# Kernel optimization log

Measured on AMD Instinct MI355X. Metric: run time of the kernel, lower is better.

## Reference

```python
import jax, jax.numpy as jnp
import numpy as np

D_MODEL = 768
NUM_HEADS = 12
SEQ_LEN = 4096
BATCH = 1


def setup_inputs() -> dict:
    key = jax.random.key(0)
    k1, k2, k3, k4 = jax.random.split(key, 4)
    x = jax.random.normal(k1, (BATCH, SEQ_LEN, D_MODEL), dtype=jnp.float32)
    # nn.Linear(d_model, 3*d_model, bias=False): store as [d_model, 3*d_model] so h = x @ w_qkv
    w_qkv = jax.random.normal(k2, (D_MODEL, 3 * D_MODEL), dtype=jnp.float32) * (1.0 / np.sqrt(D_MODEL))
    w_proj = jax.random.normal(k3, (D_MODEL, D_MODEL), dtype=jnp.float32) * (1.0 / np.sqrt(D_MODEL))
    b_proj = jax.random.normal(k4, (D_MODEL,), dtype=jnp.float32) * 0.01
    return {"x": x, "w_qkv": w_qkv, "w_proj": w_proj, "b_proj": b_proj}


def reference(x, w_qkv, w_proj, b_proj):
    n, t, c = x.shape
    H = NUM_HEADS
    dh = c // H
    # fused QKV projection: [n, t, 3c] -> per head contiguous [q|k|v] chunks of dh
    h = (x @ w_qkv).reshape(n, t, H, 3, dh)
    q = h[..., 0, :]  # [n, t, H, dh]
    k = h[..., 1, :]
    v = h[..., 2, :]
    scale = 1.0 / np.sqrt(dh)
    # full TxT score matrix, as in the hand-rolled torch module
    scores = jnp.einsum('nqhd,nkhd->nhqk', q, k) * scale  # [n, H, t, t]
    causal = jnp.tril(jnp.ones((t, t), dtype=bool))  # tril buffer
    scores = jnp.where(causal, scores, jnp.finfo(scores.dtype).min)
    att = jax.nn.softmax(scores, axis=-1)
    out = jnp.einsum('nhqk,nkhd->nqhd', att, v).reshape(n, t, c)
    return out @ w_proj + b_proj
```

## Files before the change

kernel.cpp:

```cpp
#include <hip/hip_runtime.h>

#define T_SEQ 4096
#define DM    768
#define NH    12
#define DH    64
#define NC    2304

using half8  = __attribute__((ext_vector_type(8))) _Float16;
using half4v = __attribute__((ext_vector_type(4))) _Float16;
using f32x4  = __attribute__((ext_vector_type(4))) float;
using f32x16 = __attribute__((ext_vector_type(16))) float;
typedef unsigned int u32;

union H8 { half8 v; u32 u[4]; };

__device__ __forceinline__ u32 pkrtz_u32(float a, float b) {
    return __builtin_bit_cast(u32, __builtin_amdgcn_cvt_pkrtz(a, b));
}
__device__ __forceinline__ float asf(u32 x) { return __builtin_bit_cast(float, x); }
__device__ __forceinline__ u32 asu(float x) { return __builtin_bit_cast(u32, x); }

__device__ __forceinline__ void async_copy16(void* lds, const void* g) {
    __builtin_amdgcn_global_load_lds(
        (const __attribute__((address_space(1))) u32*)g,
        (__attribute__((address_space(3))) u32*)lds, 16, 0, 0);
}

__global__ __launch_bounds__(256)
void convert_x_kernel(const float* __restrict__ x, _Float16* __restrict__ xh) {
    const size_t i = ((size_t)blockIdx.x * 256 + threadIdx.x) * 8;
    float4 a = *(const float4*)(x + i);
    float4 b = *(const float4*)(x + i + 4);
    half8 o = { (_Float16)a.x, (_Float16)a.y, (_Float16)a.z, (_Float16)a.w,
                (_Float16)b.x, (_Float16)b.y, (_Float16)b.z, (_Float16)b.w };
    *(half8*)(xh + i) = o;
}

__global__ __launch_bounds__(256)
void transpose_convert_kernel(const float* __restrict__ src,
                              _Float16* __restrict__ dst, int R, int C) {
    __shared__ _Float16 tile[64][72];
    const int tid = threadIdx.x;
    const int tc0 = blockIdx.x * 64;
    const int tr0 = blockIdx.y * 64;
    const int r = tid >> 2, c4 = (tid & 3) * 16;
    const float* sp = src + (size_t)(tr0 + r) * C + tc0 + c4;
    #pragma unroll
    for (int j = 0; j < 16; j += 4) {
        float4 t4 = *(const float4*)(sp + j);
        tile[r][c4 + j + 0] = (_Float16)t4.x;
        tile[r][c4 + j + 1] = (_Float16)t4.y;
        tile[r][c4 + j + 2] = (_Float16)t4.z;
        tile[r][c4 + j + 3] = (_Float16)t4.w;
    }
    __syncthreads();
    const int c = tid >> 2, r4 = (tid & 3) * 16;
    half8 o0, o1;
    #pragma unroll
    for (int j = 0; j < 8; ++j) o0[j] = tile[r4 + j][c];
    #pragma unroll
    for (int j = 0; j < 8; ++j) o1[j] = tile[r4 + 8 + j][c];
    _Float16* dp = dst + (size_t)(tc0 + c) * R + tr0 + r4;
    *(half8*)(dp) = o0;
    *(half8*)(dp + 8) = o1;
}

__global__ __launch_bounds__(256, 2)
void qkv_mfma_kernel(const _Float16* __restrict__ A,
                     const _Float16* __restrict__ Bt,
                     _Float16* __restrict__ q, _Float16* __restrict__ k,
                     _Float16* __restrict__ vt) {
    __shared__ _Float16 Alds[128 * 64];
    __shared__ _Float16 Blds[128 * 64];
    const int tid  = threadIdx.x;
    const int lane = tid & 63;
    const int w    = tid >> 6;
    const int wr = w >> 1, wc = w & 1;
    const int lrow = lane >> 4, lcol = lane & 15;

    const int bid  = blockIdx.x;
    const int virt = (bid & 7) * 72 + (bid >> 3);
    const int cbn  = virt % 18, rbn = virt / 18;

    const _Float16* Ag = A  + (size_t)rbn * 128 * DM;
    const _Float16* Bg = Bt + (size_t)cbn * 128 * DM;

    int srow[4], scol[4];
    #pragma unroll
    for (int i = 0; i < 4; ++i) {
        const int idx = i * 256 + tid;
        srow[i] = idx >> 3;
        scol[i] = ((idx & 7) ^ (srow[i] & 7)) * 8;
    }

    f32x4 acc[4][4];
    #pragma unroll
    for (int mf = 0; mf < 4; ++mf)
        #pragma unroll
        for (int nf = 0; nf < 4; ++nf) acc[mf][nf] = (f32x4){0.f, 0.f, 0.f, 0.f};

    for (int kt = 0; kt < DM / 64; ++kt) {
        const int k0 = kt * 64;
        __syncthreads();
        #pragma unroll
        for (int i = 0; i < 4; ++i) {
            async_copy16((char*)Alds + (i * 256 + w * 64) * 16,
                         Ag + (size_t)srow[i] * DM + k0 + scol[i]);
            async_copy16((char*)Blds + (i * 256 + w * 64) * 16,
                         Bg + (size_t)srow[i] * DM + k0 + scol[i]);
        }
        __syncthreads();
        #pragma unroll
        for (int kh = 0; kh < 2; ++kh) {
            half8 af[4], bf[4];
            const int ag = kh * 4 + lrow;
            #pragma unroll
            for (int f = 0; f < 4; ++f) {
                const int ar = wr * 64 + f * 16 + lcol;
                af[f] = *(const half8*)((const char*)Alds +
                          ar * 128 + ((ag ^ (ar & 7)) << 4));
                const int br = wc * 64 + f * 16 + lcol;
                bf[f] = *(const half8*)((const char*)Blds +
                          br * 128 + ((ag ^ (br & 7)) << 4));
            }
            #pragma unroll
            for (int mf = 0; mf < 4; ++mf)
                #pragma unroll
                for (int nf = 0; nf < 4; ++nf)
                    acc[mf][nf] = __builtin_amdgcn_mfma_f32_16x16x32_f16(
                        af[mf], bf[nf], acc[mf][nf], 0, 0, 0);
        }
    }

    #pragma unroll
    for (int nf = 0; nf < 4; ++nf) {
        const int n = cbn * 128 + wc * 64 + nf * 16 + lcol;
        const int head  = n / 192;
        const int which = (n >> 6) % 3;
        const int d = n & 63;
        if (which == 2) {
            _Float16* dv = vt + ((size_t)head * DH + d) * T_SEQ;
            #pragma unroll
            for (int mf = 0; mf < 4; ++mf) {
                const int t0 = rbn * 128 + wr * 64 + mf * 16 + lrow * 4;
                half4v o = { (_Float16)acc[mf][nf][0], (_Float16)acc[mf][nf][1],
                             (_Float16)acc[mf][nf][2], (_Float16)acc[mf][nf][3] };
                *(half4v*)(dv + t0) = o;
            }
        } else {
            _Float16* dst = (which == 0) ? q : k;
            const float sc = (which == 0) ? 0.18033688011112042f : 1.0f;
            dst += (size_t)head * T_SEQ * DH + d;
            #pragma unroll
            for (int mf = 0; mf < 4; ++mf) {
                const int t0 = rbn * 128 + wr * 64 + mf * 16 + lrow * 4;
                #pragma unroll
                for (int r = 0; r < 4; ++r)
                    dst[(size_t)(t0 + r) * DH] = (_Float16)(acc[mf][nf][r] * sc);
            }
        }
    }
}

__global__ __launch_bounds__(256, 2)
void proj_mfma_kernel(const _Float16* __restrict__ A,
                      const _Float16* __restrict__ Bt,
                      const float* __restrict__ bias, float* __restrict__ out) {
    __shared__ _Float16 Alds[128 * 64];
    __shared__ _Float16 Blds[128 * 64];
    const int tid  = threadIdx.x;
    const int lane = tid & 63;
    const int w    = tid >> 6;
    const int wr = w >> 1, wc = w & 1;
    const int lrow = lane >> 4, lcol = lane & 15;

    const int bid  = blockIdx.x;
    const int virt = (bid & 7) * 24 + (bid >> 3);
    const int cbn  = virt % 6, rbn = virt / 6;

    const _Float16* Ag = A  + (size_t)rbn * 128 * DM;
    const _Float16* Bg = Bt + (size_t)cbn * 128 * DM;

    int srow[4], scol[4];
    #pragma unroll
    for (int i = 0; i < 4; ++i) {
        const int idx = i * 256 + tid;
        srow[i] = idx >> 3;
        scol[i] = ((idx & 7) ^ (srow[i] & 7)) * 8;
    }

    f32x4 acc[4][4];
    #pragma unroll
    for (int mf = 0; mf < 4; ++mf)
        #pragma unroll
        for (int nf = 0; nf < 4; ++nf) acc[mf][nf] = (f32x4){0.f, 0.f, 0.f, 0.f};

    for (int kt = 0; kt < DM / 64; ++kt) {
        const int k0 = kt * 64;
        __syncthreads();
        #pragma unroll
        for (int i = 0; i < 4; ++i) {
            async_copy16((char*)Alds + (i * 256 + w * 64) * 16,
                         Ag + (size_t)srow[i] * DM + k0 + scol[i]);
            async_copy16((char*)Blds + (i * 256 + w * 64) * 16,
                         Bg + (size_t)srow[i] * DM + k0 + scol[i]);
        }
        __syncthreads();
        #pragma unroll
        for (int kh = 0; kh < 2; ++kh) {
            half8 af[4], bf[4];
            const int ag = kh * 4 + lrow;
            #pragma unroll
            for (int f = 0; f < 4; ++f) {
                const int ar = wr * 64 + f * 16 + lcol;
                af[f] = *(const half8*)((const char*)Alds +
                          ar * 128 + ((ag ^ (ar & 7)) << 4));
                const int br = wc * 64 + f * 16 + lcol;
                bf[f] = *(const half8*)((const char*)Blds +
                          br * 128 + ((ag ^ (br & 7)) << 4));
            }
            #pragma unroll
            for (int mf = 0; mf < 4; ++mf)
                #pragma unroll
                for (int nf = 0; nf < 4; ++nf)
                    acc[mf][nf] = __builtin_amdgcn_mfma_f32_16x16x32_f16(
                        af[mf], bf[nf], acc[mf][nf], 0, 0, 0);
        }
    }

    #pragma unroll
    for (int nf = 0; nf < 4; ++nf) {
        const int n = cbn * 128 + wc * 64 + nf * 16 + lcol;
        const float b = bias[n];
        #pragma unroll
        for (int mf = 0; mf < 4; ++mf) {
            const int t0 = rbn * 128 + wr * 64 + mf * 16 + lrow * 4;
            #pragma unroll
            for (int r = 0; r < 4; ++r)
                out[(size_t)(t0 + r) * DM + n] = acc[mf][nf][r] + b;
        }
    }
}

__global__ __launch_bounds__(256, 2)
void attn_tile_kernel(const _Float16* __restrict__ qg,
                      const _Float16* __restrict__ kg,
                      const _Float16* __restrict__ vtg,
                      _Float16* __restrict__ pO,
                      float* __restrict__ pml) {
    __shared__ _Float16 Kl[3][4096];
    __shared__ _Float16 Vl[3][4096];

    const int tid  = threadIdx.x;
    const int lane = tid & 63;
    const int w    = tid >> 6;
    const int l31  = lane & 31;
    const int hi   = lane >> 5;

    const int b = blockIdx.x;
    const int h = b % NH;
    const int i = 39 - b / NH;
    int j, seg;
    if (i < 4)       { j = i;                 seg = 0; }
    else if (i < 12) { const int t = i - 4;   j = 4  + (t >> 1); seg = t & 1; }
    else if (i < 24) { const int t = i - 12;  j = 8  + t / 3;    seg = t % 3; }
    else             { const int t = i - 24;  j = 12 + (t >> 2); seg = t & 3; }

    const int c0 = 8 * j + w;
    const int c1 = 8 * j + 4 + w;
    const int q0 = c0 * 32 + l31;
    const int q1 = c1 * 32 + l31;
    const int niter0 = c0 / 2 + 1;
    const int niter1 = c1 / 2 + 1;
    const int tS      = seg * 16;
    const int tEndBlk = min(tS + 16, 4 * j + 4);
    const int tEnd0   = min(tS + 16, niter0);
    const int tEnd1   = min(tS + 16, niter1);

    const _Float16* Kh = kg  + (size_t)h * T_SEQ * DH;
    const _Float16* Vh = vtg + (size_t)h * DH * T_SEQ;

    half8 qf0[4], qf1[4];
    {
        const _Float16* Q0 = qg + ((size_t)h * T_SEQ + q0) * DH + hi * 8;
        const _Float16* Q1 = qg + ((size_t)h * T_SEQ + q1) * DH + hi * 8;
        #pragma unroll
        for (int ks = 0; ks < 4; ++ks) {
            qf0[ks] = *(const half8*)(Q0 + ks * 16);
            qf1[ks] = *(const half8*)(Q1 + ks * 16);
        }
    }

    f32x16 oA0 = {}, oA1 = {};
    f32x16 oB0 = {}, oB1 = {};
    float l0 = 0.f, l1 = 0.f;

    const int g0 = tid, g1 = tid + 256;
    const int r0 = g0 >> 3, s0 = ((g0 & 7) ^ (r0 & 7)) * 8;
    const int r1 = g1 >> 3, s1 = ((g1 & 7) ^ (r1 & 7)) * 8;

    auto stage = [&](int p, int kvb) {
        async_copy16((char*)Kl[p] + g0 * 16, Kh + (size_t)(kvb + r0) * DH + s0);
        async_copy16((char*)Kl[p] + g1 * 16, Kh + (size_t)(kvb + r1) * DH + s1);
        async_copy16((char*)Vl[p] + g0 * 16, Vh + (size_t)r0 * T_SEQ + kvb + s0);
        async_copy16((char*)Vl[p] + g1 * 16, Vh + (size_t)r1 * T_SEQ + kvb + s1);
    };

    stage(0, tS * 64);
    stage(1, min(tS + 1, tEndBlk - 1) * 64);
    stage(2, min(tS + 2, tEndBlk - 1) * 64);

    for (int it = tS; it < tEndBlk; ++it) {
        const int p = (it - tS) % 3;

        if (it + 2 < tEndBlk) {
            asm volatile("s_waitcnt vmcnt(8)" ::: "memory");
        } else if (it + 1 < tEndBlk) {
            asm volatile("s_waitcnt vmcnt(4)" ::: "memory");
        } else {
            asm volatile("s_waitcnt vmcnt(0)" ::: "memory");
        }
        __builtin_amdgcn_s_barrier();

        if (it < tEnd1) {
            const int kvb = it * 64;
            const char* Kb = (const char*)Kl[p];
            const char* Vb = (const char*)Vl[p];
            const int sw7 = l31 & 7;

            half8 kfA[4], kfB[4];
            #pragma unroll
            for (int ks = 0; ks < 4; ++ks) {
                const int gsl = (ks * 2 + hi) ^ sw7;
                kfA[ks] = *(const half8*)(Kb + l31 * 128 + (gsl << 4));
                kfB[ks] = *(const half8*)(Kb + (32 + l31) * 128 + (gsl << 4));
            }
            half8 vf[2][2][2];
            #pragma unroll
            for (int t = 0; t < 2; ++t)
                #pragma unroll
                for (int dt = 0; dt < 2; ++dt)
                    #pragma unroll
                    for (int ks2 = 0; ks2 < 2; ++ks2) {
                        const int gsl = (t * 4 + ks2 * 2 + hi) ^ sw7;
                        vf[t][dt][ks2] = *(const half8*)(Vb +
                            (dt * 32 + l31) * 128 + (gsl << 4));
                    }

            auto run_stream = [&](const half8* qf, f32x16& o0v, f32x16& o1v,
                                  float& lsum, int qrow, int niter) {
                f32x16 sA, sB;
                #pragma unroll
                for (int r = 0; r < 16; ++r) { sA[r] = -8.0f; sB[r] = -8.0f; }
                __builtin_amdgcn_s_setprio(1);
                #pragma unroll
                for (int ks = 0; ks < 4; ++ks) {
                    sA = __builtin_amdgcn_mfma_f32_32x32x16_f16(kfA[ks], qf[ks], sA, 0, 0, 0);
                    sB = __builtin_amdgcn_mfma_f32_32x32x16_f16(kfB[ks], qf[ks], sB, 0, 0, 0);
                }
                __builtin_amdgcn_s_setprio(0);

                if (it == niter - 1) {
                    #pragma unroll
                    for (int r = 0; r < 16; ++r) {
                        const int off = (r & 3) + 8 * (r >> 2) + 4 * hi;
                        if (kvb + off > qrow)      sA[r] = -1e30f;
                        if (kvb + 32 + off > qrow) sB[r] = -1e30f;
                    }
                }

                #pragma unroll
                for (int r = 0; r < 16; ++r) sA[r] = __builtin_amdgcn_exp2f(sA[r]);
                #pragma unroll
                for (int r = 0; r < 16; ++r) sB[r] = __builtin_amdgcn_exp2f(sB[r]);
                float s8[8];
                #pragma unroll
                for (int r = 0; r < 8; ++r)
                    s8[r] = (sA[r] + sA[r + 8]) + (sB[r] + sB[r + 8]);
                float rsum = ((s8[0] + s8[4]) + (s8[1] + s8[5])) +
                             ((s8[2] + s8[6]) + (s8[3] + s8[7]));
                {
                    auto rr = __builtin_amdgcn_permlane32_swap(asu(rsum), asu(rsum), false, false);
                    rsum = asf(rr[0]) + asf(rr[1]);
                }
                lsum += rsum;

                H8 pfA[2], pfB[2];
                #pragma unroll
                for (int ks2 = 0; ks2 < 2; ++ks2) {
                    {
                        const u32 a0 = pkrtz_u32(sA[8*ks2+0], sA[8*ks2+1]);
                        const u32 a1 = pkrtz_u32(sA[8*ks2+2], sA[8*ks2+3]);
                        const u32 b0 = pkrtz_u32(sA[8*ks2+4], sA[8*ks2+5]);
                        const u32 b1 = pkrtz_u32(sA[8*ks2+6], sA[8*ks2+7]);
                        auto r0v = __builtin_amdgcn_permlane32_swap(a0, b0, false, false);
                        auto r1v = __builtin_amdgcn_permlane32_swap(a1, b1, false, false);
                        pfA[ks2].u[0] = r0v[0];
                        pfA[ks2].u[1] = r1v[0];
                        pfA[ks2].u[2] = r0v[1];
                        pfA[ks2].u[3] = r1v[1];
                    }
                    {
                        const u32 a0 = pkrtz_u32(sB[8*ks2+0], sB[8*ks2+1]);
                        const u32 a1 = pkrtz_u32(sB[8*ks2+2], sB[8*ks2+3]);
                        const u32 b0 = pkrtz_u32(sB[8*ks2+4], sB[8*ks2+5]);
                        const u32 b1 = pkrtz_u32(sB[8*ks2+6], sB[8*ks2+7]);
                        auto r0v = __builtin_amdgcn_permlane32_swap(a0, b0, false, false);
                        auto r1v = __builtin_amdgcn_permlane32_swap(a1, b1, false, false);
                        pfB[ks2].u[0] = r0v[0];
                        pfB[ks2].u[1] = r1v[0];
                        pfB[ks2].u[2] = r0v[1];
                        pfB[ks2].u[3] = r1v[1];
                    }
                }

                __builtin_amdgcn_s_setprio(1);
                #pragma unroll
                for (int ks2 = 0; ks2 < 2; ++ks2) {
                    o0v = __builtin_amdgcn_mfma_f32_32x32x16_f16(vf[0][0][ks2], pfA[ks2].v, o0v, 0, 0, 0);
                    o1v = __builtin_amdgcn_mfma_f32_32x32x16_f16(vf[0][1][ks2], pfA[ks2].v, o1v, 0, 0, 0);
                    o0v = __builtin_amdgcn_mfma_f32_32x32x16_f16(vf[1][0][ks2], pfB[ks2].v, o0v, 0, 0, 0);
                    o1v = __builtin_amdgcn_mfma_f32_32x32x16_f16(vf[1][1][ks2], pfB[ks2].v, o1v, 0, 0, 0);
                }
                __builtin_amdgcn_s_setprio(0);
            };

            if (it < tEnd0) run_stream(qf0, oA0, oA1, l0, q0, niter0);
            run_stream(qf1, oB0, oB1, l1, q1, niter1);
        }

        __builtin_amdgcn_s_barrier();
        if (it + 3 < tEndBlk) stage(p, (it + 3) * 64);
    }

    auto write_partial = [&](int c, const f32x16& o0v, const f32x16& o1v, float l) {
        const int hc = h * 128 + c;
        const float inv = (l > 0.f) ? 1.0f / l : 0.f;
        _Float16* op = pO + ((size_t)(seg * 1536 + hc) * 32 + l31) * 64 + 4 * hi;
        #pragma unroll
        for (int g = 0; g < 4; ++g) {
            half4v w0 = { (_Float16)(o0v[4*g+0] * inv), (_Float16)(o0v[4*g+1] * inv),
                          (_Float16)(o0v[4*g+2] * inv), (_Float16)(o0v[4*g+3] * inv) };
            half4v w1 = { (_Float16)(o1v[4*g+0] * inv), (_Float16)(o1v[4*g+1] * inv),
                          (_Float16)(o1v[4*g+2] * inv), (_Float16)(o1v[4*g+3] * inv) };
            *(half4v*)(op + 8 * g)      = w0;
            *(half4v*)(op + 32 + 8 * g) = w1;
        }
        if (hi == 0) {
            float* mp = pml + ((size_t)(seg * 1536 + hc) * 32 + l31) * 2;
            mp[0] = 0.0f;
            mp[1] = l;
        }
    };
    write_partial(c0, oA0, oA1, l0);
    write_partial(c1, oB0, oB1, l1);
}

__global__ __launch_bounds__(256)
void attn_combine_kernel(const _Float16* __restrict__ pO,
                         const float* __restrict__ pml,
                         _Float16* __restrict__ att) {
    const int row = blockIdx.x * 256 + threadIdx.x;
    const int q5 = row & 31;
    const int hc = row >> 5;
    const int c  = hc & 127;
    const int h  = hc >> 7;
    const int nseg = c / 32 + 1;

    float ll[4];
    float L = 0.f;
    #pragma unroll
    for (int s = 0; s < 4; ++s) {
        const bool on = s < nseg;
        const float* mp = pml + ((size_t)(s * 1536 + hc) * 32 + q5) * 2;
        ll[s] = on ? mp[1] : 0.f;
        L += ll[s];
    }
    const float invL = 1.0f / L;

    float acc[64];
    #pragma unroll
    for (int d = 0; d < 64; ++d) acc[d] = 0.f;
    #pragma unroll
    for (int s = 0; s < 4; ++s) {
        if (s >= nseg) break;
        const _Float16* src = pO + ((size_t)(s * 1536 + hc) * 32 + q5) * 64;
        const float wsc = ll[s] * invL;
        #pragma unroll
        for (int g = 0; g < 8; ++g) {
            half8 v = *(const half8*)(src + g * 8);
            #pragma unroll
            for (int jj = 0; jj < 8; ++jj)
                acc[g * 8 + jj] += wsc * (float)v[jj];
        }
    }
    _Float16* dst = att + (size_t)(c * 32 + q5) * DM + h * DH;
    #pragma unroll
    for (int g = 0; g < 8; ++g) {
        half8 o;
        #pragma unroll
        for (int jj = 0; jj < 8; ++jj) o[jj] = (_Float16)acc[g * 8 + jj];
        *(half8*)(dst + g * 8) = o;
    }
}

extern "C" void kernel_launch(void* const* d_in, const int* in_sizes, int n_in,
                              void* d_out, int out_size, void* d_ws, size_t ws_size,
                              hipStream_t stream) {
    const float* x      = (const float*)d_in[0];
    const float* w_qkv  = (const float*)d_in[1];
    const float* w_proj = (const float*)d_in[2];
    const float* b_proj = (const float*)d_in[3];
    float* out = (float*)d_out;

    _Float16* wsb = (_Float16*)d_ws;
    const size_t XS = (size_t)T_SEQ * DM;
    const size_t HS = (size_t)NH * T_SEQ * DH;
    _Float16* xh     = wsb;
    _Float16* wqkvT  = xh + XS;
    _Float16* wprojT = wqkvT + (size_t)NC * DM;
    _Float16* q      = wprojT + (size_t)DM * DM;
    _Float16* k      = q + HS;
    _Float16* vt     = k + HS;
    _Float16* att    = vt + HS;
    _Float16* pO     = att + XS;
    float*    pml    = (float*)(pO + (size_t)4 * 1536 * 32 * 64);

    convert_x_kernel<<<dim3(1536), 256, 0, stream>>>(x, xh);
    transpose_convert_kernel<<<dim3(36, 12), 256, 0, stream>>>(w_qkv, wqkvT, DM, NC);
    transpose_convert_kernel<<<dim3(12, 12), 256, 0, stream>>>(w_proj, wprojT, DM, DM);
    qkv_mfma_kernel<<<dim3(576), 256, 0, stream>>>(xh, wqkvT, q, k, vt);
    attn_tile_kernel<<<dim3(480), 256, 0, stream>>>(q, k, vt, pO, pml);
    attn_combine_kernel<<<dim3(192), 256, 0, stream>>>(pO, pml, att);
    proj_mfma_kernel<<<dim3(192), 256, 0, stream>>>(att, wprojT, b_proj, out);
}
```

Baseline: 104.9 us.

## Merge prep kernels and retile QKV and projection GEMMs for better wave fill

Folds the x conversion and both weight transposes into a single prep kernel, removing two launches. Changes the QKV GEMM to 128x192 tiles over 384 blocks so each block covers one head's q|k|v columns and reuses A across more columns. Halves the projection GEMM row tile to 64, doubling its grid to 384 blocks to fill more CUs. This adds LDS and accumulator register pressure in the QKV kernel, and the smaller projection tile reuses each B tile across fewer rows.

Measured after the change: 97.17 us (median of 2 runs). -7.4%, faster.

```diff
diff --git a/kernel.cpp b/kernel.cpp
--- a/kernel.cpp
+++ b/kernel.cpp
@@ -27,22 +27,35 @@
 }
 
 __global__ __launch_bounds__(256)
-void convert_x_kernel(const float* __restrict__ x, _Float16* __restrict__ xh) {
-    const size_t i = ((size_t)blockIdx.x * 256 + threadIdx.x) * 8;
-    float4 a = *(const float4*)(x + i);
-    float4 b = *(const float4*)(x + i + 4);
-    half8 o = { (_Float16)a.x, (_Float16)a.y, (_Float16)a.z, (_Float16)a.w,
-                (_Float16)b.x, (_Float16)b.y, (_Float16)b.z, (_Float16)b.w };
-    *(half8*)(xh + i) = o;
-}
-
-__global__ __launch_bounds__(256)
-void transpose_convert_kernel(const float* __restrict__ src,
-                              _Float16* __restrict__ dst, int R, int C) {
+void prep_kernel(const float* __restrict__ x, _Float16* __restrict__ xh,
+                 const float* __restrict__ w_qkv, _Float16* __restrict__ wqkvT,
+                 const float* __restrict__ w_proj, _Float16* __restrict__ wprojT) {
     __shared__ _Float16 tile[64][72];
+    const int b = blockIdx.x;
     const int tid = threadIdx.x;
-    const int tc0 = blockIdx.x * 64;
-    const int tr0 = blockIdx.y * 64;
+
+    if (b < 1536) {
+        const size_t i = ((size_t)b * 256 + tid) * 8;
+        float4 a = *(const float4*)(x + i);
+        float4 c = *(const float4*)(x + i + 4);
+        half8 o = { (_Float16)a.x, (_Float16)a.y, (_Float16)a.z, (_Float16)a.w,
+                    (_Float16)c.x, (_Float16)c.y, (_Float16)c.z, (_Float16)c.w };
+        *(half8*)(xh + i) = o;
+        return;
+    }
+
+    const float* src;
+    _Float16* dst;
+    int R, C, tc0, tr0;
+    if (b < 1968) {
+        const int b2 = b - 1536;
+        src = w_qkv; dst = wqkvT; R = DM; C = NC;
+        tc0 = (b2 % 36) * 64; tr0 = (b2 / 36) * 64;
+    } else {
+        const int b3 = b - 1968;
+        src = w_proj; dst = wprojT; R = DM; C = DM;
+        tc0 = (b3 % 12) * 64; tr0 = (b3 / 12) * 64;
+    }
     const int r = tid >> 2, c4 = (tid & 3) * 16;
     const float* sp = src + (size_t)(tr0 + r) * C + tc0 + c4;
     #pragma unroll
@@ -71,6 +84,112 @@
                      _Float16* __restrict__ q, _Float16* __restrict__ k,
                      _Float16* __restrict__ vt) {
     __shared__ _Float16 Alds[128 * 64];
+    __shared__ _Float16 Blds[192 * 64];
+    const int tid  = threadIdx.x;
+    const int lane = tid & 63;
+    const int w    = tid >> 6;
+    const int wr = w >> 1, wc = w & 1;
+    const int lrow = lane >> 4, lcol = lane & 15;
+
+    const int bid  = blockIdx.x;
+    const int virt = (bid & 7) * 48 + (bid >> 3);
+    const int cbn  = virt % 12, rbn = virt / 12;
+
+    const _Float16* Ag = A  + (size_t)rbn * 128 * DM;
+    const _Float16* Bg = Bt + (size_t)cbn * 192 * DM;
+
+    int srA[4], scA[4], srB[6], scB[6];
+    #pragma unroll
+    for (int i = 0; i < 4; ++i) {
+        const int idx = i * 256 + tid;
+        srA[i] = idx >> 3;
+        scA[i] = ((idx & 7) ^ (srA[i] & 7)) * 8;
+    }
+    #pragma unroll
+    for (int i = 0; i < 6; ++i) {
+        const int idx = i * 256 + tid;
+        srB[i] = idx >> 3;
+        scB[i] = ((idx & 7) ^ (srB[i] & 7)) * 8;
+    }
+
+    f32x4 acc[4][6];
+    #pragma unroll
+    for (int mf = 0; mf < 4; ++mf)
+        #pragma unroll
+        for (int nf = 0; nf < 6; ++nf) acc[mf][nf] = (f32x4){0.f, 0.f, 0.f, 0.f};
+
+    for (int kt = 0; kt < DM / 64; ++kt) {
+        const int k0 = kt * 64;
+        __syncthreads();
+        #pragma unroll
+        for (int i = 0; i < 4; ++i)
+            async_copy16((char*)Alds + (i * 256 + tid) * 16,
+                         Ag + (size_t)srA[i] * DM + k0 + scA[i]);
+        #pragma unroll
+        for (int i = 0; i < 6; ++i)
+            async_copy16((char*)Blds + (i * 256 + tid) * 16,
+                         Bg + (size_t)srB[i] * DM + k0 + scB[i]);
+        __syncthreads();
+        #pragma unroll
+        for (int kh = 0; kh < 2; ++kh) {
+            half8 af[4], bf[6];
+            const int ag = kh * 4 + lrow;
+            #pragma unroll
+            for (int f = 0; f < 4; ++f) {
+                const int ar = wr * 64 + f * 16 + lcol;
+                af[f] = *(const half8*)((const char*)Alds +
+                          ar * 128 + ((ag ^ (ar & 7)) << 4));
+            }
+            #pragma unroll
+            for (int f = 0; f < 6; ++f) {
+                const int br = wc * 96 + f * 16 + lcol;
+                bf[f] = *(const half8*)((const char*)Blds +
+                          br * 128 + ((ag ^ (br & 7)) << 4));
+            }
+            #pragma unroll
+            for (int mf = 0; mf < 4; ++mf)
+                #pragma unroll
+                for (int nf = 0; nf < 6; ++nf)
+                    acc[mf][nf] = __builtin_amdgcn_mfma_f32_16x16x32_f16(
+                        af[mf], bf[nf], acc[mf][nf], 0, 0, 0);
+        }
+    }
+
+    #pragma unroll
+    for (int nf = 0; nf < 6; ++nf) {
+        const int n = cbn * 192 + wc * 96 + nf * 16 + lcol;
+        const int head  = n / 192;
+        const int which = (n >> 6) % 3;
+        const int d = n & 63;
+        if (which == 2) {
+            _Float16* dv = vt + ((size_t)head * DH + d) * T_SEQ;
+            #pragma unroll
+            for (int mf = 0; mf < 4; ++mf) {
+                const int t0 = rbn * 128 + wr * 64 + mf * 16 + lrow * 4;
+                half4v o = { (_Float16)acc[mf][nf][0], (_Float16)acc[mf][nf][1],
+                             (_Float16)acc[mf][nf][2], (_Float16)acc[mf][nf][3] };
+                *(half4v*)(dv + t0) = o;
+            }
+        } else {
+            _Float16* dst = (which == 0) ? q : k;
+            const float sc = (which == 0) ? 0.18033688011112042f : 1.0f;
+            dst += (size_t)head * T_SEQ * DH + d;
+            #pragma unroll
+            for (int mf = 0; mf < 4; ++mf) {
+                const int t0 = rbn * 128 + wr * 64 + mf * 16 + lrow * 4;
+                #pragma unroll
+                for (int r = 0; r < 4; ++r)
+                    dst[(size_t)(t0 + r) * DH] = (_Float16)(acc[mf][nf][r] * sc);
+            }
+        }
+    }
+}
+
+__global__ __launch_bounds__(256, 2)
+void proj_mfma_kernel(const _Float16* __restrict__ A,
+                      const _Float16* __restrict__ Bt,
+                      const float* __restrict__ bias, float* __restrict__ out) {
+    __shared__ _Float16 Alds[64 * 64];
     __shared__ _Float16 Blds[128 * 64];
     const int tid  = threadIdx.x;
     const int lane = tid & 63;
@@ -79,23 +198,29 @@
     const int lrow = lane >> 4, lcol = lane & 15;
 
     const int bid  = blockIdx.x;
-    const int virt = (bid & 7) * 72 + (bid >> 3);
-    const int cbn  = virt % 18, rbn = virt / 18;
-
-    const _Float16* Ag = A  + (size_t)rbn * 128 * DM;
+    const int virt = (bid & 7) * 48 + (bid >> 3);
+    const int cbn  = virt % 6, rbn = virt / 6;
+
+    const _Float16* Ag = A  + (size_t)rbn * 64 * DM;
     const _Float16* Bg = Bt + (size_t)cbn * 128 * DM;
 
-    int srow[4], scol[4];
+    int srA[2], scA[2], srB[4], scB[4];
+    #pragma unroll
+    for (int i = 0; i < 2; ++i) {
+        const int idx = i * 256 + tid;
+        srA[i] = idx >> 3;
+        scA[i] = ((idx & 7) ^ (srA[i] & 7)) * 8;
+    }
     #pragma unroll
     for (int i = 0; i < 4; ++i) {
         const int idx = i * 256 + tid;
-        srow[i] = idx >> 3;
-        scol[i] = ((idx & 7) ^ (srow[i] & 7)) * 8;
-    }
-
-    f32x4 acc[4][4];
-    #pragma unroll
-    for (int mf = 0; mf < 4; ++mf)
+        srB[i] = idx >> 3;
+        scB[i] = ((idx & 7) ^ (srB[i] & 7)) * 8;
+    }
+
+    f32x4 acc[2][4];
+    #pragma unroll
+    for (int mf = 0; mf < 2; ++mf)
         #pragma unroll
         for (int nf = 0; nf < 4; ++nf) acc[mf][nf] = (f32x4){0.f, 0.f, 0.f, 0.f};
 
@@ -103,28 +228,32 @@
         const int k0 = kt * 64;
         __syncthreads();
         #pragma unroll
-        for (int i = 0; i < 4; ++i) {
-            async_copy16((char*)Alds + (i * 256 + w * 64) * 16,
-                         Ag + (size_t)srow[i] * DM + k0 + scol[i]);
-            async_copy16((char*)Blds + (i * 256 + w * 64) * 16,
-                         Bg + (size_t)srow[i] * DM + k0 + scol[i]);
-        }
+        for (int i = 0; i < 2; ++i)
+            async_copy16((char*)Alds + (i * 256 + tid) * 16,
+                         Ag + (size_t)srA[i] * DM + k0 + scA[i]);
+        #pragma unroll
+        for (int i = 0; i < 4; ++i)
+            async_copy16((char*)Blds + (i * 256 + tid) * 16,
+                         Bg + (size_t)srB[i] * DM + k0 + scB[i]);
         __syncthreads();
         #pragma unroll
         for (int kh = 0; kh < 2; ++kh) {
-            half8 af[4], bf[4];
+            half8 af[2], bf[4];
             const int ag = kh * 4 + lrow;
             #pragma unroll
-            for (int f = 0; f < 4; ++f) {
-                const int ar = wr * 64 + f * 16 + lcol;
+            for (int f = 0; f < 2; ++f) {
+                const int ar = wr * 32 + f * 16 + lcol;
                 af[f] = *(const half8*)((const char*)Alds +
                           ar * 128 + ((ag ^ (ar & 7)) << 4));
+            }
+            #pragma unroll
+            for (int f = 0; f < 4; ++f) {
                 const int br = wc * 64 + f * 16 + lcol;
                 bf[f] = *(const half8*)((const char*)Blds +
                           br * 128 + ((ag ^ (br & 7)) << 4));
             }
             #pragma unroll
-            for (int mf = 0; mf < 4; ++mf)
+            for (int mf = 0; mf < 2; ++mf)
                 #pragma unroll
                 for (int nf = 0; nf < 4; ++nf)
                     acc[mf][nf] = __builtin_amdgcn_mfma_f32_16x16x32_f16(
@@ -135,106 +264,10 @@
     #pragma unroll
     for (int nf = 0; nf < 4; ++nf) {
         const int n = cbn * 128 + wc * 64 + nf * 16 + lcol;
-        const int head  = n / 192;
-        const int which = (n >> 6) % 3;
-        const int d = n & 63;
-        if (which == 2) {
-            _Float16* dv = vt + ((size_t)head * DH + d) * T_SEQ;
-            #pragma unroll
-            for (int mf = 0; mf < 4; ++mf) {
-                const int t0 = rbn * 128 + wr * 64 + mf * 16 + lrow * 4;
-                half4v o = { (_Float16)acc[mf][nf][0], (_Float16)acc[mf][nf][1],
-                             (_Float16)acc[mf][nf][2], (_Float16)acc[mf][nf][3] };
-                *(half4v*)(dv + t0) = o;
-            }
-        } else {
-            _Float16* dst = (which == 0) ? q : k;
-            const float sc = (which == 0) ? 0.18033688011112042f : 1.0f;
-            dst += (size_t)head * T_SEQ * DH + d;
-            #pragma unroll
-            for (int mf = 0; mf < 4; ++mf) {
-                const int t0 = rbn * 128 + wr * 64 + mf * 16 + lrow * 4;
-                #pragma unroll
-                for (int r = 0; r < 4; ++r)
-                    dst[(size_t)(t0 + r) * DH] = (_Float16)(acc[mf][nf][r] * sc);
-            }
-        }
-    }
-}
-
-__global__ __launch_bounds__(256, 2)
-void proj_mfma_kernel(const _Float16* __restrict__ A,
-                      const _Float16* __restrict__ Bt,
-                      const float* __restrict__ bias, float* __restrict__ out) {
-    __shared__ _Float16 Alds[128 * 64];
-    __shared__ _Float16 Blds[128 * 64];
-    const int tid  = threadIdx.x;
-    const int lane = tid & 63;
-    const int w    = tid >> 6;
-    const int wr = w >> 1, wc = w & 1;
-    const int lrow = lane >> 4, lcol = lane & 15;
-
-    const int bid  = blockIdx.x;
-    const int virt = (bid & 7) * 24 + (bid >> 3);
-    const int cbn  = virt % 6, rbn = virt / 6;
-
-    const _Float16* Ag = A  + (size_t)rbn * 128 * DM;
-    const _Float16* Bg = Bt + (size_t)cbn * 128 * DM;
-
-    int srow[4], scol[4];
-    #pragma unroll
-    for (int i = 0; i < 4; ++i) {
-        const int idx = i * 256 + tid;
-        srow[i] = idx >> 3;
-        scol[i] = ((idx & 7) ^ (srow[i] & 7)) * 8;
-    }
-
-    f32x4 acc[4][4];
-    #pragma unroll
-    for (int mf = 0; mf < 4; ++mf)
-        #pragma unroll
-        for (int nf = 0; nf < 4; ++nf) acc[mf][nf] = (f32x4){0.f, 0.f, 0.f, 0.f};
-
-    for (int kt = 0; kt < DM / 64; ++kt) {
-        const int k0 = kt * 64;
-        __syncthreads();
-        #pragma unroll
-        for (int i = 0; i < 4; ++i) {
-            async_copy16((char*)Alds + (i * 256 + w * 64) * 16,
-                         Ag + (size_t)srow[i] * DM + k0 + scol[i]);
-            async_copy16((char*)Blds + (i * 256 + w * 64) * 16,
-                         Bg + (size_t)srow[i] * DM + k0 + scol[i]);
-        }
-        __syncthreads();
-        #pragma unroll
-        for (int kh = 0; kh < 2; ++kh) {
-            half8 af[4], bf[4];
-            const int ag = kh * 4 + lrow;
-            #pragma unroll
-            for (int f = 0; f < 4; ++f) {
-                const int ar = wr * 64 + f * 16 + lcol;
-                af[f] = *(const half8*)((const char*)Alds +
-                          ar * 128 + ((ag ^ (ar & 7)) << 4));
-                const int br = wc * 64 + f * 16 + lcol;
-                bf[f] = *(const half8*)((const char*)Blds +
-                          br * 128 + ((ag ^ (br & 7)) << 4));
-            }
-            #pragma unroll
-            for (int mf = 0; mf < 4; ++mf)
-                #pragma unroll
-                for (int nf = 0; nf < 4; ++nf)
-                    acc[mf][nf] = __builtin_amdgcn_mfma_f32_16x16x32_f16(
-                        af[mf], bf[nf], acc[mf][nf], 0, 0, 0);
-        }
-    }
-
-    #pragma unroll
-    for (int nf = 0; nf < 4; ++nf) {
-        const int n = cbn * 128 + wc * 64 + nf * 16 + lcol;
         const float b = bias[n];
         #pragma unroll
-        for (int mf = 0; mf < 4; ++mf) {
-            const int t0 = rbn * 128 + wr * 64 + mf * 16 + lrow * 4;
+        for (int mf = 0; mf < 2; ++mf) {
+            const int t0 = rbn * 64 + wr * 32 + mf * 16 + lrow * 4;
             #pragma unroll
             for (int r = 0; r < 4; ++r)
                 out[(size_t)(t0 + r) * DM + n] = acc[mf][nf][r] + b;
@@ -526,11 +559,9 @@
     _Float16* pO     = att + XS;
     float*    pml    = (float*)(pO + (size_t)4 * 1536 * 32 * 64);
 
-    convert_x_kernel<<<dim3(1536), 256, 0, stream>>>(x, xh);
-    transpose_convert_kernel<<<dim3(36, 12), 256, 0, stream>>>(w_qkv, wqkvT, DM, NC);
-    transpose_convert_kernel<<<dim3(12, 12), 256, 0, stream>>>(w_proj, wprojT, DM, DM);
-    qkv_mfma_kernel<<<dim3(576), 256, 0, stream>>>(xh, wqkvT, q, k, vt);
+    prep_kernel<<<dim3(2112), 256, 0, stream>>>(x, xh, w_qkv, wqkvT, w_proj, wprojT);
+    qkv_mfma_kernel<<<dim3(384), 256, 0, stream>>>(xh, wqkvT, q, k, vt);
     attn_tile_kernel<<<dim3(480), 256, 0, stream>>>(q, k, vt, pO, pml);
     attn_combine_kernel<<<dim3(192), 256, 0, stream>>>(pO, pml, att);
-    proj_mfma_kernel<<<dim3(192), 256, 0, stream>>>(att, wprojT, b_proj, out);
-}
+    proj_mfma_kernel<<<dim3(384), 256, 0, stream>>>(att, wprojT, b_proj, out);
+}
```
